# Performance work log

Measured on AMD Instinct MI355X. Metric: run time of the kernel, lower is better.

## Reference

```python
import jax, jax.numpy as jnp
import numpy as np

EMBED = 512
H = 8
HD = EMBED // H           # 64
NUM_CLS = 4
WIN = 32                  # one-sided window radius
DIL = 1
WLEN = 2 * WIN + 1        # 65
CTX = NUM_CLS + WLEN      # 69
PATCH_LEN = 8192
B = 1
S = NUM_CLS + PATCH_LEN
THETA = 10000.0
COORD_HIGH = 100000.0
NEG = -1e30


def _rotate_half(x):
    # [..., x1, x2, ...] -> [..., -x2, x1, ...]
    x1 = x[..., 0::2]
    x2 = x[..., 1::2]
    return jnp.stack([-x2, x1], axis=-1).reshape(x.shape)


def _rope2d(x, coords):
    # x: (B,H,L,HD), coords: (B,L,2)
    half = HD // 2
    inv_freq = 1.0 / (THETA ** (jnp.arange(0, half, 2, dtype=jnp.float32) / half))  # (half//2,)
    xy = coords / COORD_HIGH
    fx = xy[..., 0][..., None] * inv_freq   # (B,L,half//2)
    fy = xy[..., 1][..., None] * inv_freq
    fx = jnp.repeat(fx, 2, axis=-1)         # (B,L,half)
    fy = jnp.repeat(fy, 2, axis=-1)
    freqs = jnp.concatenate([fx, fy], axis=-1)[:, None]  # (B,1,L,HD)
    return x * jnp.cos(freqs) + _rotate_half(x) * jnp.sin(freqs)


def setup_inputs() -> dict:
    key = jax.random.key(0)
    k1, k2, k3, k4, k5, k6 = jax.random.split(key, 6)
    x = jax.random.normal(k1, (B, S, EMBED), dtype=jnp.float32)
    coords = jax.random.uniform(k2, (B, PATCH_LEN, 2), dtype=jnp.float32) * COORD_HIGH
    sc = 1.0 / np.sqrt(EMBED)
    w_qkv = jax.random.normal(k3, (3 * EMBED, EMBED), dtype=jnp.float32) * sc
    b_qkv = jax.random.normal(k4, (3 * EMBED,), dtype=jnp.float32) * 0.02
    w_out = jax.random.normal(k5, (EMBED, EMBED), dtype=jnp.float32) * sc
    b_out = jax.random.normal(k6, (EMBED,), dtype=jnp.float32) * 0.02
    return {"x": x, "coords": coords, "w_qkv": w_qkv, "b_qkv": b_qkv,
            "w_out": w_out, "b_out": b_out}


def _forward(x, coords, w_qkv, b_qkv, w_out, b_out):
    Bb, seq_len, _ = x.shape
    qkv = x @ w_qkv.T + b_qkv                       # (B,S,3E)
    qkv = qkv.reshape(Bb, seq_len, 3, H, HD)
    qkv = jnp.transpose(qkv, (2, 0, 3, 1, 4))       # (3,B,H,S,HD)
    q, k, v = qkv[0], qkv[1], qkv[2]
    q_cls, k_cls, v_cls = q[:, :, :NUM_CLS], k[:, :, :NUM_CLS], v[:, :, :NUM_CLS]
    q_p, k_p, v_p = q[:, :, NUM_CLS:], k[:, :, NUM_CLS:], v[:, :, NUM_CLS:]

    q_p = _rope2d(q_p, coords)
    k_p = _rope2d(k_p, coords)
    k_all = jnp.concatenate([k_cls, k_p], axis=2)
    v_all = v

    scale = 1.0 / np.sqrt(HD)

    # --- global CLS attention: CLS queries attend to everything ---
    cls_scores = jnp.einsum('bhqd,bhkd->bhqk', q_cls, k_all) * scale
    cls_probs = jax.nn.softmax(cls_scores, axis=-1)
    cls_out = jnp.einsum('bhqk,bhkd->bhqd', cls_probs, v_all)

    # --- windowed patch attention: patch i -> [CLS | patches i-W..i+W (dilated)] ---
    L = PATCH_LEN
    pad = WIN * DIL
    k_pad = jnp.pad(k_p, ((0, 0), (0, 0), (pad, pad), (0, 0)))
    v_pad = jnp.pad(v_p, ((0, 0), (0, 0), (pad, pad), (0, 0)))
    gather_idx = jnp.arange(L)[:, None] + jnp.arange(WLEN)[None, :] * DIL  # (L,WLEN)
    k_win = k_pad[:, :, gather_idx]   # (B,H,L,WLEN,HD)
    v_win = v_pad[:, :, gather_idx]

    s_cls = jnp.einsum('bhld,bhcd->bhlc', q_p, k_cls) * scale     # (B,H,L,NUM_CLS)
    s_win = jnp.einsum('bhld,bhlwd->bhlw', q_p, k_win) * scale    # (B,H,L,WLEN)

    pos = jnp.arange(L)[:, None] + (jnp.arange(WLEN)[None, :] - WIN) * DIL
    in_bounds = (pos >= 0) & (pos < L)                            # (L,WLEN)
    s_win = jnp.where(in_bounds[None, None], s_win, NEG)

    scores = jnp.concatenate([s_cls, s_win], axis=-1)             # (B,H,L,CTX)
    probs = jax.nn.softmax(scores, axis=-1)
    p_cls, p_win = probs[..., :NUM_CLS], probs[..., NUM_CLS:]
    patch_out = (jnp.einsum('bhlc,bhcd->bhld', p_cls, v_cls)
                 + jnp.einsum('bhlw,bhlwd->bhld', p_win, v_win))

    out = jnp.concatenate([cls_out, patch_out], axis=2)           # (B,H,S,HD)
    out = jnp.transpose(out, (0, 2, 1, 3)).reshape(Bb, seq_len, EMBED)
    return out @ w_out.T + b_out


def reference(x, coords, w_qkv, b_qkv, w_out, b_out):
    return _forward(x, coords, w_qkv, b_qkv, w_out, b_out)
```

## Files before the change

### kernel.cpp

```cpp
#include <hip/hip_runtime.h>
#include <math.h>

#define EMBED 512
#define NHEAD 8
#define HD 64
#define NUM_CLS 4
#define WIN 32
#define WLEN 65
#define PATCH_LEN 8192
#define S_TOT 8196
#define QKV_LD 1536
#define VT_LD 8200

typedef short bf16x8 __attribute__((ext_vector_type(8)));
typedef float f32x4 __attribute__((ext_vector_type(4)));

__device__ __forceinline__ unsigned short f2bf(float f) {
    unsigned u = __float_as_uint(f);
    return (unsigned short)((u + 0x7fffu + ((u >> 16) & 1u)) >> 16);
}
__device__ __forceinline__ float bf2f(unsigned short v) {
    return __uint_as_float((unsigned)v << 16);
}

__global__ __launch_bounds__(256) void cast_all(const float* __restrict__ x,
                                                const float* __restrict__ wq,
                                                const float* __restrict__ wo,
                                                unsigned short* __restrict__ xb,
                                                unsigned short* __restrict__ wqb,
                                                unsigned short* __restrict__ wob)
{
    const int n1 = S_TOT * EMBED;
    const int n2 = 3 * EMBED * EMBED;
    const int n3 = EMBED * EMBED;
    const int i = (blockIdx.x * 256 + threadIdx.x) * 4;
    const float* src;
    unsigned short* dst;
    int j;
    if (i < n1)           { src = x;  dst = xb;  j = i; }
    else if (i < n1 + n2) { src = wq; dst = wqb; j = i - n1; }
    else if (i < n1 + n2 + n3) { src = wo; dst = wob; j = i - n1 - n2; }
    else return;
    const float4 v = *(const float4*)(src + j);
    ushort4 o;
    o.x = f2bf(v.x); o.y = f2bf(v.y); o.z = f2bf(v.z); o.w = f2bf(v.w);
    *(ushort4*)(dst + j) = o;
}

template <int MODE, typename OutT>
__global__ __launch_bounds__(256) void gemm_bf16_nt(const unsigned short* __restrict__ A,
                                                    const unsigned short* __restrict__ B,
                                                    const float* __restrict__ bias,
                                                    OutT* __restrict__ C,
                                                    int M, int N, int K,
                                                    const float* __restrict__ coords,
                                                    unsigned short* __restrict__ vT)
{
    __shared__ __align__(16) unsigned short As[128 * 32];
    __shared__ __align__(16) unsigned short Bs[128 * 32];
    const int tid = threadIdx.x;
    const int lane = tid & 63, w = tid >> 6;
    const int bm = blockIdx.x, bn = blockIdx.y;

    const int ar0 = tid >> 2;
    const int col8 = (tid & 3) * 8;
    int gm0 = bm * 128 + ar0;       if (gm0 >= M) gm0 = M - 1;
    int gm1 = bm * 128 + ar0 + 64;  if (gm1 >= M) gm1 = M - 1;
    const int gn0 = bn * 128 + ar0;
    const int gn1 = bn * 128 + ar0 + 64;
    const unsigned short* pa0 = A + (size_t)gm0 * K + col8;
    const unsigned short* pa1 = A + (size_t)gm1 * K + col8;
    const unsigned short* pb0 = B + (size_t)gn0 * K + col8;
    const unsigned short* pb1 = B + (size_t)gn1 * K + col8;
    unsigned short* la0 = As + tid * 8;
    unsigned short* la1 = As + (tid + 256) * 8;
    unsigned short* lb0 = Bs + tid * 8;
    unsigned short* lb1 = Bs + (tid + 256) * 8;

    const int wr = (w & 1) * 64;
    const int wc = (w >> 1) * 64;
    const int fr = lane & 15;
    const int fk = (lane >> 4) * 8;

    f32x4 acc[4][4];
#pragma unroll
    for (int mi = 0; mi < 4; ++mi)
#pragma unroll
        for (int ni = 0; ni < 4; ++ni) acc[mi][ni] = (f32x4)0.f;

    for (int k0 = 0; k0 < K; k0 += 32) {
        __builtin_amdgcn_global_load_lds((const __attribute__((address_space(1))) void*)(pa0 + k0),
                                         (__attribute__((address_space(3))) void*)la0, 16, 0, 0);
        __builtin_amdgcn_global_load_lds((const __attribute__((address_space(1))) void*)(pa1 + k0),
                                         (__attribute__((address_space(3))) void*)la1, 16, 0, 0);
        __builtin_amdgcn_global_load_lds((const __attribute__((address_space(1))) void*)(pb0 + k0),
                                         (__attribute__((address_space(3))) void*)lb0, 16, 0, 0);
        __builtin_amdgcn_global_load_lds((const __attribute__((address_space(1))) void*)(pb1 + k0),
                                         (__attribute__((address_space(3))) void*)lb1, 16, 0, 0);
        __syncthreads();

        bf16x8 af[4], bf[4];
#pragma unroll
        for (int mi = 0; mi < 4; ++mi)
            af[mi] = *(const bf16x8*)(As + (wr + mi * 16 + fr) * 32 + fk);
#pragma unroll
        for (int ni = 0; ni < 4; ++ni)
            bf[ni] = *(const bf16x8*)(Bs + (wc + ni * 16 + fr) * 32 + fk);
#pragma unroll
        for (int mi = 0; mi < 4; ++mi)
#pragma unroll
            for (int ni = 0; ni < 4; ++ni)
                acc[mi][ni] = __builtin_amdgcn_mfma_f32_16x16x32_bf16(af[mi], bf[ni], acc[mi][ni], 0, 0, 0);
        __syncthreads();
    }

    const int ccol = bn * 128 + wc + fr;

    if constexpr (MODE == 0) {
#pragma unroll
        for (int mi = 0; mi < 4; ++mi) {
            const int rbase = bm * 128 + wr + mi * 16 + (lane >> 4) * 4;
#pragma unroll
            for (int r = 0; r < 4; ++r) {
                const int row = rbase + r;
                if (row < M) {
#pragma unroll
                    for (int ni = 0; ni < 4; ++ni)
                        C[(size_t)row * N + ccol + ni * 16] = acc[mi][ni][r] + bias[ccol + ni * 16];
                }
            }
        }
    } else {
        if (bn < 8) {
#pragma unroll
            for (int mi = 0; mi < 4; ++mi) {
                const int rbase = bm * 128 + wr + mi * 16 + (lane >> 4) * 4;
#pragma unroll
                for (int r = 0; r < 4; ++r) {
                    const int row = rbase + r;
                    const bool patch = (row >= NUM_CLS) && (row < M);
                    float cx = 0.f, cy = 0.f;
                    if (patch) {
                        const int l = row - NUM_CLS;
                        cx = coords[l * 2 + 0] * 1e-5f;
                        cy = coords[l * 2 + 1] * 1e-5f;
                    }
#pragma unroll
                    for (int ni = 0; ni < 4; ++ni) {
                        const int col = ccol + ni * 16;
                        const float biased = acc[mi][ni][r] + bias[col];
                        const float part = __shfl_xor(biased, 1);
                        float outv = biased;
                        if (patch) {
                            const int dh = col & 63;
                            const int pr = dh >> 1;
                            const float invf = __expf(-(float)(pr & 15) * 0.5756462732485114f);
                            const float f = ((pr < 16) ? cx : cy) * invf;
                            float sn, cs;
                            __sincosf(f, &sn, &cs);
                            outv = (dh & 1) ? (biased * cs + part * sn)
                                            : (biased * cs - part * sn);
                        }
                        if (row < M) C[(size_t)row * N + col] = (OutT)f2bf(outv);
                    }
                }
            }
        } else {
#pragma unroll
            for (int mi = 0; mi < 4; ++mi) {
                const int rbase = bm * 128 + wr + mi * 16 + (lane >> 4) * 4;
#pragma unroll
                for (int ni = 0; ni < 4; ++ni) {
                    const int col = ccol + ni * 16;
                    const int dv = col - 1024;
                    unsigned short b[4];
#pragma unroll
                    for (int r = 0; r < 4; ++r)
                        b[r] = f2bf(acc[mi][ni][r] + bias[col]);
#pragma unroll
                    for (int r = 0; r < 4; ++r)
                        if (rbase + r < M) C[(size_t)(rbase + r) * N + col] = (OutT)b[r];
                    if (rbase + 3 < M) {
                        ushort4 o; o.x = b[0]; o.y = b[1]; o.z = b[2]; o.w = b[3];
                        *(ushort4*)(vT + (size_t)dv * VT_LD + rbase) = o;
                    } else {
#pragma unroll
                        for (int r = 0; r < 4; ++r) {
                            const int row = rbase + r;
                            if (row < VT_LD)
                                vT[(size_t)dv * VT_LD + row] = (row < M) ? b[r] : (unsigned short)0;
                        }
                    }
                }
            }
        }
    }
}

#define CCH 128
#define NCHUNK ((S_TOT + CCH - 1) / CCH)
#define PSTRIDE 68

__global__ __launch_bounds__(256) void cls_attn_partial(const unsigned short* __restrict__ qkv,
                                                        float* __restrict__ part)
{
    const int h = blockIdx.x;
    const int c = blockIdx.y;
    const int tid = threadIdx.x;
    const int base = c * CCH;

    __shared__ float qs[4][64];
    __shared__ float sc[4][CCH];
    __shared__ float ored[4][4][64];
    __shared__ float ml[4][2];

    {
        const int qi = tid >> 6, d = tid & 63;
        qs[qi][d] = bf2f(qkv[(size_t)qi * QKV_LD + h * HD + d]);
    }
    __syncthreads();

    {
        const int jj = tid & 127;
        const int qp = (tid >> 7) * 2;
        const int j = base + jj;
        float s0 = -INFINITY, s1 = -INFINITY;
        if (j < S_TOT) {
            const unsigned short* kp = qkv + (size_t)j * QKV_LD + EMBED + h * HD;
            float a0 = 0.f, a1 = 0.f;
#pragma unroll
            for (int d8 = 0; d8 < 64; d8 += 8) {
                const bf16x8 kv8 = *(const bf16x8*)(kp + d8);
#pragma unroll
                for (int u = 0; u < 8; ++u) {
                    const float kf = bf2f((unsigned short)kv8[u]);
                    a0 += qs[qp + 0][d8 + u] * kf;
                    a1 += qs[qp + 1][d8 + u] * kf;
                }
            }
            s0 = a0 * 0.125f; s1 = a1 * 0.125f;
        }
        sc[qp + 0][jj] = s0;
        sc[qp + 1][jj] = s1;
    }
    __syncthreads();

    const int w = tid >> 6, lane = tid & 63;
    {
        float m = fmaxf(sc[w][lane], sc[w][lane + 64]);
#pragma unroll
        for (int off = 32; off > 0; off >>= 1) m = fmaxf(m, __shfl_xor(m, off, 64));
        const float e0 = expf(sc[w][lane] - m);
        const float e1 = expf(sc[w][lane + 64] - m);
        sc[w][lane] = e0; sc[w][lane + 64] = e1;
        float lsum = e0 + e1;
#pragma unroll
        for (int off = 32; off > 0; off >>= 1) lsum += __shfl_xor(lsum, off, 64);
        if (lane == 0) { ml[w][0] = m; ml[w][1] = lsum; }
    }
    __syncthreads();

    {
        const int g = w, d = lane;
        float a0 = 0.f, a1 = 0.f, a2 = 0.f, a3 = 0.f;
        for (int jj = g; jj < CCH; jj += 4) {
            const int j = base + jj;
            if (j >= S_TOT) break;
            const float vv = bf2f(qkv[(size_t)j * QKV_LD + 2 * EMBED + h * HD + d]);
            a0 += sc[0][jj] * vv; a1 += sc[1][jj] * vv;
            a2 += sc[2][jj] * vv; a3 += sc[3][jj] * vv;
        }
        ored[g][0][d] = a0; ored[g][1][d] = a1; ored[g][2][d] = a2; ored[g][3][d] = a3;
    }
    __syncthreads();

    {
        const int qi = tid >> 6, d = tid & 63;
        const float o = ored[0][qi][d] + ored[1][qi][d] + ored[2][qi][d] + ored[3][qi][d];
        float* pb = part + ((size_t)(h * NCHUNK + c) * 4 + qi) * PSTRIDE;
        pb[d] = o;
        if (d == 0) { pb[64] = ml[qi][0]; pb[65] = ml[qi][1]; }
    }
}

__global__ __launch_bounds__(256) void cls_attn_combine(const float* __restrict__ part,
                                                        unsigned short* __restrict__ attn)
{
    const int h = blockIdx.x;
    const int qi = threadIdx.x >> 6, d = threadIdx.x & 63;
    float M = -INFINITY;
    for (int c = 0; c < NCHUNK; ++c)
        M = fmaxf(M, part[((size_t)(h * NCHUNK + c) * 4 + qi) * PSTRIDE + 64]);
    float acc = 0.f, L = 0.f;
    for (int c = 0; c < NCHUNK; ++c) {
        const float* pb = part + ((size_t)(h * NCHUNK + c) * 4 + qi) * PSTRIDE;
        const float s = expf(pb[64] - M);
        acc += s * pb[d];
        L   += s * pb[65];
    }
    attn[(size_t)qi * EMBED + h * HD + d] = f2bf(acc / L);
}

#define SW 116
#define PW 136

__global__ __launch_bounds__(256) void patch_attn_mfma(
    const unsigned short* __restrict__ qkv,
    const unsigned short* __restrict__ vT,
    unsigned short* __restrict__ attnb)
{
    const int l0 = blockIdx.x * 32;
    const int h = blockIdx.y;
    const int tid = threadIdx.x;
    const int lane = tid & 63, w = tid >> 6;

    __shared__ __align__(16) unsigned short Qs[32 * 64];
    __shared__ __align__(16) unsigned short Ks[112 * 64];
    __shared__ __align__(16) unsigned short Vt[64 * 128];
    __shared__ __align__(16) float Sm[32 * SW];

    {
        const int i = tid;
        const int t = i >> 3;
        const int dcl = (i & 7) ^ (t & 7);
        const unsigned short* g = qkv + (size_t)(NUM_CLS + l0 + t) * QKV_LD + h * HD + dcl * 8;
        __builtin_amdgcn_global_load_lds((const __attribute__((address_space(1))) void*)g,
                                         (__attribute__((address_space(3))) void*)(Qs + i * 8), 16, 0, 0);
    }
    for (int i = tid; i < 896; i += 256) {
        const int c = i >> 3;
        const int dcl = (i & 7) ^ (c & 7);
        int tok = (c >= 104 && c < 108) ? (c - 104) : (l0 - 32 + c);
        tok = tok < 0 ? 0 : (tok > S_TOT - 1 ? S_TOT - 1 : tok);
        const unsigned short* g = qkv + (size_t)tok * QKV_LD + EMBED + h * HD + dcl * 8;
        __builtin_amdgcn_global_load_lds((const __attribute__((address_space(1))) void*)g,
                                         (__attribute__((address_space(3))) void*)(Ks + i * 8), 16, 0, 0);
    }
    for (int i = tid; i < 1024; i += 256) {
        const int d = i >> 4;
        const int kcl = (i & 15) ^ (d & 15);
        const int c0 = kcl * 8;
        int tokb = (c0 == 104) ? 0 : (l0 - 32 + c0);
        tokb = tokb < 0 ? 0 : (tokb > 8192 ? 8192 : tokb);
        const unsigned short* g = vT + (size_t)(h * HD + d) * VT_LD + tokb;
        __builtin_amdgcn_global_load_lds((const __attribute__((address_space(1))) void*)g,
                                         (__attribute__((address_space(3))) void*)(Vt + i * 8), 16, 0, 0);
    }
    __syncthreads();

    bf16x8 qf[2][2];
#pragma unroll
    for (int mt = 0; mt < 2; ++mt)
#pragma unroll
        for (int ks = 0; ks < 2; ++ks) {
            const int row = mt * 16 + (lane & 15);
            const int dc = (ks * 4 + (lane >> 4)) ^ (row & 7);
            qf[mt][ks] = *(const bf16x8*)(Qs + row * 64 + dc * 8);
        }
    for (int idx = w; idx < 14; idx += 4) {
        const int mt = idx & 1, nt = idx >> 1;
        f32x4 acc = (f32x4)0.f;
#pragma unroll
        for (int ks = 0; ks < 2; ++ks) {
            const int kr = nt * 16 + (lane & 15);
            const int dc = (ks * 4 + (lane >> 4)) ^ (kr & 7);
            const bf16x8 kf = *(const bf16x8*)(Ks + kr * 64 + dc * 8);
            acc = __builtin_amdgcn_mfma_f32_16x16x32_bf16(qf[mt][ks], kf, acc, 0, 0, 0);
        }
        const int col = nt * 16 + (lane & 15);
        const int r0 = mt * 16 + (lane >> 4) * 4;
#pragma unroll
        for (int r = 0; r < 4; ++r) Sm[(r0 + r) * SW + col] = acc[r];
    }
    __syncthreads();

    {
        const int t = tid >> 3, lq = tid & 7;
        float e[14];
        float m = -INFINITY;
#pragma unroll
        for (int j = 0; j < 14; ++j) {
            const int c = lq + 8 * j;
            bool valid;
            if (c >= 104) valid = (c < 108);
            else {
                const int r = c - 4;
                const int pos = l0 - 32 + r;
                valid = (c >= 4) && (c < 100) && (r >= t) && (r <= t + 64) &&
                        (pos >= 0) && (pos < PATCH_LEN);
            }
            e[j] = valid ? Sm[t * SW + c] * 0.125f : -INFINITY;
            m = fmaxf(m, e[j]);
        }
#pragma unroll
        for (int off = 1; off < 8; off <<= 1) m = fmaxf(m, __shfl_xor(m, off, 64));
        float sum = 0.f;
#pragma unroll
        for (int j = 0; j < 14; ++j) { e[j] = expf(e[j] - m); sum += e[j]; }
#pragma unroll
        for (int off = 1; off < 8; off <<= 1) sum += __shfl_xor(sum, off, 64);
        const float inv = 1.f / sum;
        __syncthreads();
        unsigned short* P = (unsigned short*)Sm;
#pragma unroll
        for (int j = 0; j < 14; ++j) P[t * PW + lq + 8 * j] = f2bf(e[j] * inv);
        ushort2 z; z.x = 0; z.y = 0;
        *(ushort2*)(P + (tid >> 3) * PW + 112 + (tid & 7) * 2) = z;
    }
    __syncthreads();

    {
        const unsigned short* P = (const unsigned short*)Sm;
        const int mt = w & 1;
        bf16x8 pf[4];
#pragma unroll
        for (int ks = 0; ks < 4; ++ks) {
            const int row = mt * 16 + (lane & 15);
            pf[ks] = *(const bf16x8*)(P + row * PW + ks * 32 + (lane >> 4) * 8);
        }
#pragma unroll
        for (int nn = 0; nn < 2; ++nn) {
            const int nt = (w >> 1) + nn * 2;
            f32x4 acc = (f32x4)0.f;
#pragma unroll
            for (int ks = 0; ks < 4; ++ks) {
                const int d = nt * 16 + (lane & 15);
                const int kc = (ks * 4 + (lane >> 4)) ^ (d & 15);
                const bf16x8 vf = *(const bf16x8*)(Vt + d * 128 + kc * 8);
                acc = __builtin_amdgcn_mfma_f32_16x16x32_bf16(pf[ks], vf, acc, 0, 0, 0);
            }
            const int dcol = nt * 16 + (lane & 15);
            const int r0 = mt * 16 + (lane >> 4) * 4;
#pragma unroll
            for (int r = 0; r < 4; ++r)
                attnb[(size_t)(NUM_CLS + l0 + r0 + r) * EMBED + h * HD + dcol] = f2bf(acc[r]);
        }
    }
}

extern "C" void kernel_launch(void* const* d_in, const int* in_sizes, int n_in,
                              void* d_out, int out_size, void* d_ws, size_t ws_size,
                              hipStream_t stream)
{
    const float* x      = (const float*)d_in[0];
    const float* coords = (const float*)d_in[1];
    const float* w_qkv  = (const float*)d_in[2];
    const float* b_qkv  = (const float*)d_in[3];
    const float* w_out  = (const float*)d_in[4];
    const float* b_out  = (const float*)d_in[5];
    float* out = (float*)d_out;

    char* p = (char*)d_ws;
    unsigned short* qkv   = (unsigned short*)p;  p += (size_t)S_TOT * QKV_LD * 2;
    unsigned short* vT    = (unsigned short*)p;  p += (size_t)EMBED * VT_LD * 2;
    unsigned short* attnb = (unsigned short*)p;  p += (size_t)S_TOT * EMBED * 2;
    float*          part  = (float*)p;           p += (size_t)NHEAD * NCHUNK * 4 * PSTRIDE * 4;
    unsigned short* wob   = (unsigned short*)p;  p += (size_t)EMBED * EMBED * 2;
    unsigned short* xb    = (unsigned short*)p;  p += (size_t)S_TOT * EMBED * 2;
    unsigned short* wqb   = (unsigned short*)p;


    {
        const int total = S_TOT * EMBED + 3 * EMBED * EMBED + EMBED * EMBED;
        cast_all<<<(total / 4 + 255) / 256, 256, 0, stream>>>(x, w_qkv, w_out, xb, wqb, wob);
    }

    gemm_bf16_nt<1, unsigned short><<<dim3((S_TOT + 127) / 128, (3 * EMBED) / 128), 256, 0, stream>>>(
        xb, wqb, b_qkv, qkv, S_TOT, 3 * EMBED, EMBED, coords, vT);

    cls_attn_partial<<<dim3(NHEAD, NCHUNK), 256, 0, stream>>>(qkv, part);
    cls_attn_combine<<<NHEAD, 256, 0, stream>>>(part, attnb);

    patch_attn_mfma<<<dim3(PATCH_LEN / 32, NHEAD), 256, 0, stream>>>(qkv, vT, attnb);

    gemm_bf16_nt<0, float><<<dim3((S_TOT + 127) / 128, EMBED / 128), 256, 0, stream>>>(
        attnb, wob, b_out, out, S_TOT, EMBED, EMBED, nullptr, nullptr);
}
```

Before: 196.3 us.

## Stage RoPE table, V transpose and CLS keys through LDS; swap GEMM grid order

The QKV GEMM epilogue now precomputes a per-tile cos/sin RoPE table in shared memory instead of calling sincos per element. It also writes the V transpose through an LDS staging buffer so that the vT stores are wide and coalesced rather than 4-element scattered. The CLS partial-attention kernel loads its key chunk into swizzled LDS with global_load_lds before the dot products. Both GEMM grids swap x/y so blocks sharing the same A rows run adjacently for better cache reuse. The costs are extra shared memory, more syncs in the epilogue, and bf16 rounding of the cos/sin values.

```diff
diff --git a/kernel.cpp b/kernel.cpp
--- a/kernel.cpp
+++ b/kernel.cpp
@@ -60,7 +60,7 @@
     __shared__ __align__(16) unsigned short Bs[128 * 32];
     const int tid = threadIdx.x;
     const int lane = tid & 63, w = tid >> 6;
-    const int bm = blockIdx.x, bn = blockIdx.y;
+    const int bn = blockIdx.x, bm = blockIdx.y;
 
     const int ar0 = tid >> 2;
     const int col8 = (tid & 3) * 8;
@@ -131,66 +131,94 @@
             }
         }
     } else {
+        __shared__ __align__(16) unsigned short EX[64 * 136];
         if (bn < 8) {
+            ushort2* rt = (ushort2*)EX;
+            for (int idx = tid; idx < 4096; idx += 256) {
+                const int rr = idx >> 5, pr = idx & 31;
+                int l = bm * 128 + rr - NUM_CLS;
+                l = l < 0 ? 0 : (l > PATCH_LEN - 1 ? PATCH_LEN - 1 : l);
+                const float cxy = coords[l * 2 + (pr >> 4)] * 1e-5f;
+                const float f = cxy * __expf(-(float)(pr & 15) * 0.5756462732485114f);
+                float sn, cs;
+                __sincosf(f, &sn, &cs);
+                ushort2 e; e.x = f2bf(cs); e.y = f2bf(sn);
+                rt[idx] = e;
+            }
+            __syncthreads();
 #pragma unroll
             for (int mi = 0; mi < 4; ++mi) {
-                const int rbase = bm * 128 + wr + mi * 16 + (lane >> 4) * 4;
+                const int rloc0 = wr + mi * 16 + (lane >> 4) * 4;
 #pragma unroll
                 for (int r = 0; r < 4; ++r) {
-                    const int row = rbase + r;
+                    const int rloc = rloc0 + r;
+                    const int row = bm * 128 + rloc;
                     const bool patch = (row >= NUM_CLS) && (row < M);
-                    float cx = 0.f, cy = 0.f;
-                    if (patch) {
-                        const int l = row - NUM_CLS;
-                        cx = coords[l * 2 + 0] * 1e-5f;
-                        cy = coords[l * 2 + 1] * 1e-5f;
-                    }
 #pragma unroll
                     for (int ni = 0; ni < 4; ++ni) {
                         const int col = ccol + ni * 16;
                         const float biased = acc[mi][ni][r] + bias[col];
-                        const float part = __shfl_xor(biased, 1);
+                        const float prt = __shfl_xor(biased, 1);
                         float outv = biased;
                         if (patch) {
-                            const int dh = col & 63;
-                            const int pr = dh >> 1;
-                            const float invf = __expf(-(float)(pr & 15) * 0.5756462732485114f);
-                            const float f = ((pr < 16) ? cx : cy) * invf;
-                            float sn, cs;
-                            __sincosf(f, &sn, &cs);
-                            outv = (dh & 1) ? (biased * cs + part * sn)
-                                            : (biased * cs - part * sn);
+                            const ushort2 e = rt[rloc * 32 + ((col & 63) >> 1)];
+                            const float cs = bf2f(e.x), sn = bf2f(e.y);
+                            outv = (col & 1) ? (biased * cs + prt * sn)
+                                             : (biased * cs - prt * sn);
                         }
                         if (row < M) C[(size_t)row * N + col] = (OutT)f2bf(outv);
                     }
                 }
             }
         } else {
+            const int dbase = (bn - 8) * 128;
 #pragma unroll
             for (int mi = 0; mi < 4; ++mi) {
                 const int rbase = bm * 128 + wr + mi * 16 + (lane >> 4) * 4;
 #pragma unroll
                 for (int ni = 0; ni < 4; ++ni) {
                     const int col = ccol + ni * 16;
-                    const int dv = col - 1024;
-                    unsigned short b[4];
-#pragma unroll
-                    for (int r = 0; r < 4; ++r)
-                        b[r] = f2bf(acc[mi][ni][r] + bias[col]);
-#pragma unroll
-                    for (int r = 0; r < 4; ++r)
-                        if (rbase + r < M) C[(size_t)(rbase + r) * N + col] = (OutT)b[r];
-                    if (rbase + 3 < M) {
-                        ushort4 o; o.x = b[0]; o.y = b[1]; o.z = b[2]; o.w = b[3];
-                        *(ushort4*)(vT + (size_t)dv * VT_LD + rbase) = o;
-                    } else {
-#pragma unroll
-                        for (int r = 0; r < 4; ++r) {
-                            const int row = rbase + r;
-                            if (row < VT_LD)
-                                vT[(size_t)dv * VT_LD + row] = (row < M) ? b[r] : (unsigned short)0;
+#pragma unroll
+                    for (int r = 0; r < 4; ++r) {
+                        const int row = rbase + r;
+                        if (row < M)
+                            C[(size_t)row * N + col] = (OutT)f2bf(acc[mi][ni][r] + bias[col]);
+                    }
+                }
+            }
+            for (int p = 0; p < 2; ++p) {
+                __syncthreads();
+                if ((w >> 1) == p) {
+#pragma unroll
+                    for (int mi = 0; mi < 4; ++mi) {
+                        const int tok0 = wr + mi * 16 + (lane >> 4) * 4;
+                        const int rw = bm * 128 + tok0;
+#pragma unroll
+                        for (int ni = 0; ni < 4; ++ni) {
+                            const int col = ccol + ni * 16;
+                            const int dloc = fr + 16 * ni;
+                            ushort4 o;
+                            o.x = (rw + 0 < M) ? f2bf(acc[mi][ni][0] + bias[col]) : (unsigned short)0;
+                            o.y = (rw + 1 < M) ? f2bf(acc[mi][ni][1] + bias[col]) : (unsigned short)0;
+                            o.z = (rw + 2 < M) ? f2bf(acc[mi][ni][2] + bias[col]) : (unsigned short)0;
+                            o.w = (rw + 3 < M) ? f2bf(acc[mi][ni][3] + bias[col]) : (unsigned short)0;
+                            *(ushort4*)(EX + dloc * 136 + tok0) = o;
                         }
                     }
+                }
+                __syncthreads();
+                const int d = tid >> 2;
+                const int tch = (tid & 3) * 32;
+                const int gtok = bm * 128 + tch;
+                unsigned short* dst = vT + (size_t)(dbase + p * 64 + d) * VT_LD + gtok;
+                const unsigned short* srcl = EX + d * 136 + tch;
+                if (gtok + 32 <= VT_LD) {
+#pragma unroll
+                    for (int c2 = 0; c2 < 32; c2 += 8)
+                        *(bf16x8*)(dst + c2) = *(const bf16x8*)(srcl + c2);
+                } else {
+                    for (int c2 = 0; c2 < 32; ++c2)
+                        if (gtok + c2 < VT_LD) dst[c2] = srcl[c2];
                 }
             }
         }
@@ -210,6 +238,7 @@
     const int base = c * CCH;
 
     __shared__ float qs[4][64];
+    __shared__ __align__(16) unsigned short Kl[128 * 64];
     __shared__ float sc[4][CCH];
     __shared__ float ored[4][4][64];
     __shared__ float ml[4][2];
@@ -217,6 +246,14 @@
     {
         const int qi = tid >> 6, d = tid & 63;
         qs[qi][d] = bf2f(qkv[(size_t)qi * QKV_LD + h * HD + d]);
+    }
+    for (int i = tid; i < 1024; i += 256) {
+        const int kr = i >> 3;
+        const int dc = (i & 7) ^ (kr & 7);
+        int j = base + kr; if (j > S_TOT - 1) j = S_TOT - 1;
+        const unsigned short* g = qkv + (size_t)j * QKV_LD + EMBED + h * HD + dc * 8;
+        __builtin_amdgcn_global_load_lds((const __attribute__((address_space(1))) void*)g,
+                                         (__attribute__((address_space(3))) void*)(Kl + i * 8), 16, 0, 0);
     }
     __syncthreads();
 
@@ -226,16 +263,16 @@
         const int j = base + jj;
         float s0 = -INFINITY, s1 = -INFINITY;
         if (j < S_TOT) {
-            const unsigned short* kp = qkv + (size_t)j * QKV_LD + EMBED + h * HD;
             float a0 = 0.f, a1 = 0.f;
 #pragma unroll
-            for (int d8 = 0; d8 < 64; d8 += 8) {
-                const bf16x8 kv8 = *(const bf16x8*)(kp + d8);
+            for (int cch = 0; cch < 8; ++cch) {
+                const int slot = cch ^ (jj & 7);
+                const bf16x8 kv8 = *(const bf16x8*)(Kl + jj * 64 + slot * 8);
 #pragma unroll
                 for (int u = 0; u < 8; ++u) {
                     const float kf = bf2f((unsigned short)kv8[u]);
-                    a0 += qs[qp + 0][d8 + u] * kf;
-                    a1 += qs[qp + 1][d8 + u] * kf;
+                    a0 += qs[qp + 0][cch * 8 + u] * kf;
+                    a1 += qs[qp + 1][cch * 8 + u] * kf;
                 }
             }
             s0 = a0 * 0.125f; s1 = a1 * 0.125f;
@@ -465,7 +502,7 @@
         cast_all<<<(total / 4 + 255) / 256, 256, 0, stream>>>(x, w_qkv, w_out, xb, wqb, wob);
     }
 
-    gemm_bf16_nt<1, unsigned short><<<dim3((S_TOT + 127) / 128, (3 * EMBED) / 128), 256, 0, stream>>>(
+    gemm_bf16_nt<1, unsigned short><<<dim3((3 * EMBED) / 128, (S_TOT + 127) / 128), 256, 0, stream>>>(
         xb, wqb, b_qkv, qkv, S_TOT, 3 * EMBED, EMBED, coords, vT);
 
     cls_attn_partial<<<dim3(NHEAD, NCHUNK), 256, 0, stream>>>(qkv, part);
@@ -473,6 +510,6 @@
 
     patch_attn_mfma<<<dim3(PATCH_LEN / 32, NHEAD), 256, 0, stream>>>(qkv, vT, attnb);
 
-    gemm_bf16_nt<0, float><<<dim3((S_TOT + 127) / 128, EMBED / 128), 256, 0, stream>>>(
+    gemm_bf16_nt<0, float><<<dim3(EMBED / 128, (S_TOT + 127) / 128), 256, 0, stream>>>(
         attnb, wob, b_out, out, S_TOT, EMBED, EMBED, nullptr, nullptr);
 }
```

Result: no change. 195.6 us (-0.4%).
